# Kernel tuning notes

Hardware: AMD Instinct MI355X
Metric: run time of the kernel (lower is better)

Reference implementation:

```python
import jax, jax.numpy as jnp
import numpy as np

N_NONZERO = 32      # n_nonzero_coefs
TAU = 0.01
LAMBDA_INIT = -5.0  # reg_coeff = softplus(lambda)


def setup_inputs() -> dict:
    key = jax.random.key(0)
    k1, k2 = jax.random.split(key)
    X = jax.random.normal(k1, (64, 1024, 1024), dtype=jnp.float32)
    y = jax.random.normal(k2, (64, 1024, 1), dtype=jnp.float32)
    return {"X": X, "y": y}


def _omp_fit_forward(X, y):
    # Faithful translation of fit() (omp with hard straight-through top-1)
    # followed by forward() reconstruction D @ coef.
    reg = jax.nn.softplus(jnp.asarray(LAMBDA_INIT, jnp.float32)).astype(X.dtype)
    B, L, A = X.shape
    ones = jnp.ones((B, L, 1), X.dtype)
    Dfull = jnp.concatenate([X, ones], axis=-1)   # [B, L, A+1] (bias column)
    D = Dfull[0]                                   # shared dictionary [L, A+1]
    n_atoms = A + 1
    y2 = y[:, :, 0]                                # [B, L]
    y_det = jax.lax.stop_gradient(y2)
    residuals = y_det
    # Cache selected_D columns incrementally: each column j is dict @ ret_j,
    # identical math to the original's full recompute every iteration.
    selD = jnp.zeros((B, L, N_NONZERO), X.dtype)
    idx_all = []
    nzW = None
    for i in range(N_NONZERO):
        proj = residuals @ D                                      # [B, A+1]
        soft = jax.nn.softmax(jnp.abs(proj) / TAU, axis=-1)
        idx = jnp.argmax(jnp.abs(proj), axis=-1)                  # detached indices
        onehot = jax.nn.one_hot(jnp.argmax(soft, axis=-1), n_atoms, dtype=X.dtype)
        ret = onehot - jax.lax.stop_gradient(soft) + soft         # straight-through
        new_col = ret @ D.T                                       # [B, L]
        selD = selD.at[:, :, i].set(new_col)
        Di = selD[:, :, :i + 1]                                   # [B, L, i+1]
        DTy = jnp.einsum('blk,bl->bk', Di, y2)[..., None]         # [B, i+1, 1]
        DTD = jnp.einsum('blk,blj->bkj', Di, Di) + reg * jnp.eye(i + 1, dtype=X.dtype)
        nzW = jnp.linalg.solve(DTD, DTy)                          # [B, i+1, 1]
        residuals = y_det - jnp.einsum('blk,bk->bl', Di, nzW[..., 0])
        idx_all.append(idx)
    indices = jnp.stack(idx_all, axis=1)                          # [B, K] int
    W = jnp.zeros((B, n_atoms), X.dtype).at[jnp.arange(B)[:, None], indices].set(nzW[..., 0])
    # forward(): bmm(dict_with_bias, coef)
    recon = jnp.einsum('bla,ba->bl', Dfull, W)[..., None]         # [B, L, 1]
    return recon


def reference(X, y):
    return _omp_fit_forward(X, y)
```

## Files before the change

kernel.cpp:

```cpp
#include <hip/hip_runtime.h>
#include <math.h>

#define NATOMS   1025
#define GSTRIDE  1040
#define GELEMS   (1025*GSTRIDE)
#define NNZ      32
#define NBATCH   64
#define REGL     0.0067153485f

#define DPPF(x, ctrl) __int_as_float(__builtin_amdgcn_update_dpp(0, __float_as_int(x), (ctrl), 0xF, 0xF, false))

__device__ __forceinline__ float wave_max64(float x) {
    x = fmaxf(x, DPPF(x, 0x111));
    x = fmaxf(x, DPPF(x, 0x112));
    x = fmaxf(x, DPPF(x, 0x114));
    x = fmaxf(x, DPPF(x, 0x118));
    x = fmaxf(x, DPPF(x, 0x142));
    x = fmaxf(x, DPPF(x, 0x143));
    return __int_as_float(__builtin_amdgcn_readlane(__float_as_int(x), 63));
}
__device__ __forceinline__ float wave_sum64(float x) {
    x += DPPF(x, 0x111);
    x += DPPF(x, 0x112);
    x += DPPF(x, 0x114);
    x += DPPF(x, 0x118);
    x += DPPF(x, 0x142);
    x += DPPF(x, 0x143);
    return __int_as_float(__builtin_amdgcn_readlane(__float_as_int(x), 63));
}
__device__ __forceinline__ float readlane_f(float x, int l) {
    return __int_as_float(__builtin_amdgcn_readlane(__float_as_int(x), l));
}

__global__ __launch_bounds__(256)
void gramprojy_kernel(const float* __restrict__ X0, const float* __restrict__ y,
                      float* __restrict__ Gout, float* __restrict__ PY,
                      int kLen, int nsplit) {
    __shared__ float lds[8192];
    const int tid = threadIdx.x;

    if ((int)blockIdx.z < nsplit) {
        const int bx = blockIdx.x, by = blockIdx.y, bz = blockIdx.z;
        if (by < bx) return;
        float* As = lds;
        float* Bs = lds + 4096;
        const int a0 = bx * 128, b0 = by * 128;
        float* __restrict__ Gp = Gout + (size_t)bz * GELEMS;
        const int tx = tid & 15;
        const int ty = tid >> 4;
        const int lr = tid >> 5;
        const int lc = (tid & 31) * 4;
        const bool aIn = (a0 + 128) <= 1024;
        const bool bIn = (b0 + 128) <= 1024;

        float acc[8][8];
#pragma unroll
        for (int m = 0; m < 8; ++m)
#pragma unroll
            for (int n = 0; n < 8; ++n) acc[m][n] = 0.0f;

        const int kBase = bz * kLen;
        for (int kc = 0; kc < kLen; kc += 32) {
#pragma unroll
            for (int rr = 0; rr < 4; ++rr) {
                const int r = lr + rr * 8;
                const int l = kBase + kc + r;
                if (aIn) {
                    *(float4*)&As[r * 128 + lc] = *(const float4*)&X0[(size_t)l * 1024 + a0 + lc];
                } else {
#pragma unroll
                    for (int k = 0; k < 4; ++k) {
                        const int col = a0 + lc + k;
                        As[r * 128 + lc + k] = (col < 1024) ? X0[(size_t)l * 1024 + col]
                                                            : (col == 1024 ? 1.0f : 0.0f);
                    }
                }
                if (bIn) {
                    *(float4*)&Bs[r * 128 + lc] = *(const float4*)&X0[(size_t)l * 1024 + b0 + lc];
                } else {
#pragma unroll
                    for (int k = 0; k < 4; ++k) {
                        const int col = b0 + lc + k;
                        Bs[r * 128 + lc + k] = (col < 1024) ? X0[(size_t)l * 1024 + col]
                                                            : (col == 1024 ? 1.0f : 0.0f);
                    }
                }
            }
            __syncthreads();
#pragma unroll 8
            for (int l = 0; l < 32; ++l) {
                float4 a01 = *(const float4*)&As[l * 128 + ty * 8];
                float4 a23 = *(const float4*)&As[l * 128 + ty * 8 + 4];
                float4 bA  = *(const float4*)&Bs[l * 128 + tx * 4];
                float4 bB  = *(const float4*)&Bs[l * 128 + 64 + tx * 4];
                float am[8] = {a01.x, a01.y, a01.z, a01.w, a23.x, a23.y, a23.z, a23.w};
                float bn[8] = {bA.x, bA.y, bA.z, bA.w, bB.x, bB.y, bB.z, bB.w};
#pragma unroll
                for (int m = 0; m < 8; ++m)
#pragma unroll
                    for (int n = 0; n < 8; ++n)
                        acc[m][n] += am[m] * bn[n];
            }
            __syncthreads();
        }

#pragma unroll
        for (int m = 0; m < 8; ++m) {
            const int a = a0 + ty * 8 + m;
            if (a >= NATOMS) continue;
            const int bAc = b0 + tx * 4;
            const int bBc = b0 + 64 + tx * 4;
            if (bAc < GSTRIDE) {
                *(float4*)&Gp[(size_t)a * GSTRIDE + bAc] =
                    make_float4(acc[m][0], acc[m][1], acc[m][2], acc[m][3]);
            }
            if (bBc < GSTRIDE) {
                *(float4*)&Gp[(size_t)a * GSTRIDE + bBc] =
                    make_float4(acc[m][4], acc[m][5], acc[m][6], acc[m][7]);
            }
        }
        if (bx != by) {
#pragma unroll
            for (int n = 0; n < 8; ++n) {
                const int colg = b0 + ((n < 4) ? (tx * 4 + n) : (64 + tx * 4 + (n - 4)));
                if (colg >= NATOMS) continue;
                const int a = a0 + ty * 8;
                *(float4*)&Gp[(size_t)colg * GSTRIDE + a] =
                    make_float4(acc[0][n], acc[1][n], acc[2][n], acc[3][n]);
                *(float4*)&Gp[(size_t)colg * GSTRIDE + a + 4] =
                    make_float4(acc[4][n], acc[5][n], acc[6][n], acc[7][n]);
            }
        }
    } else {
        const int pw = blockIdx.y * 9 + blockIdx.x;
        if (pw >= 68) return;
        const int a0 = (pw % 17) * 64;
        const int b0 = (pw / 17) * 16;
        float* Ds = lds;
        float* Ys = lds + 2048;
        const int tx = tid & 15;
        const int ty = tid >> 4;
        const bool aIn = (a0 + 64) <= 1024;

        float acc[4] = {0.0f, 0.0f, 0.0f, 0.0f};

        for (int kc = 0; kc < 1024; kc += 32) {
            {
                const int r  = tid >> 4;
                const int c4 = (tid & 15) * 4;
#pragma unroll
                for (int rr = 0; rr < 2; ++rr) {
                    const int row = r + rr * 16;
                    const int l = kc + row;
                    if (aIn) {
                        *(float4*)&Ds[row * 64 + c4] = *(const float4*)&X0[(size_t)l * 1024 + a0 + c4];
                    } else {
#pragma unroll
                        for (int k = 0; k < 4; ++k) {
                            const int col = a0 + c4 + k;
                            Ds[row * 64 + c4 + k] = (col < 1024) ? X0[(size_t)l * 1024 + col]
                                                                 : (col == 1024 ? 1.0f : 0.0f);
                        }
                    }
                }
            }
            for (int e = tid; e < 512; e += 256) {
                const int l = e & 31, bb = e >> 5;
                Ys[l * 17 + bb] = y[(size_t)(b0 + bb) * 1024 + kc + l];
            }
            __syncthreads();
#pragma unroll 8
            for (int l = 0; l < 32; ++l) {
                const float yv = Ys[l * 17 + ty];
                float4 dv = *(const float4*)&Ds[l * 64 + tx * 4];
                acc[0] += yv * dv.x; acc[1] += yv * dv.y;
                acc[2] += yv * dv.z; acc[3] += yv * dv.w;
            }
            __syncthreads();
        }
        const int a = a0 + tx * 4;
        if (a < GSTRIDE) {
            *(float4*)&PY[(size_t)(b0 + ty) * GSTRIDE + a] =
                make_float4(acc[0], acc[1], acc[2], acc[3]);
        }
    }
}

template <int NS>
__global__ __launch_bounds__(512)
void omp_kernel(const float* __restrict__ Gp, const float* __restrict__ PY,
                int* __restrict__ idxOut, float* __restrict__ wOut) {
    __shared__ float pyLds[1040];
    __shared__ float diagLds[1040];
    __shared__ float bvec[32];
    __shared__ float row1024[NNZ];
    __shared__ float redV[2][8];
    __shared__ int   redI[2][8];

    const int b = blockIdx.x, tid = threadIdx.x;
    const int lane = tid & 63, wid = tid >> 6;

    float rr0[NNZ], rr1[NNZ];
    float ainv[32];
#pragma unroll
    for (int m = 0; m < 32; ++m) { ainv[m] = 0.f; rr0[m] = 0.f; rr1[m] = 0.f; }
    float wvr = 0.f, rhsr = 0.f;
    int   myIdx = 0;

    {
        const float* pyg = PY + (size_t)b * GSTRIDE;
        pyLds[tid] = pyg[tid];
        pyLds[tid + 512] = pyg[tid + 512];
        if (tid < 16) pyLds[1024 + tid] = pyg[1024 + tid];
        float d0 = 0.f, d1 = 0.f, d2 = 0.f;
#pragma unroll
        for (int z = 0; z < NS; ++z) {
            const float* gz = Gp + (size_t)z * GELEMS;
            d0 += gz[(size_t)tid * (GSTRIDE + 1)];
            d1 += gz[(size_t)(tid + 512) * (GSTRIDE + 1)];
            if (tid == 511) d2 += gz[(size_t)1024 * (GSTRIDE + 1)];
        }
        diagLds[tid] = d0;
        diagLds[tid + 512] = d1;
        if (tid == 511) diagLds[1024] = d2;
        if (tid < 32) { bvec[tid] = 0.f; row1024[tid] = 0.f; }
    }
    __syncthreads();

    float p0 = pyLds[tid], p1 = pyLds[tid + 512];
    float p2 = (tid == 511) ? pyLds[1024] : 0.f;

    {
        float best = fabsf(p0); int bidx = tid;
        { float v = fabsf(p1); if (v > best) { best = v; bidx = tid + 512; } }
        if (tid == 511) { float v = fabsf(p2); if (v > best) { best = v; bidx = 1024; } }
        const float wmax = wave_max64(best);
        const unsigned long long mask = __ballot(best == wmax);
        const int fl = __ffsll((unsigned long long)mask) - 1;
        const int widx = __builtin_amdgcn_readlane(bidx, fl);
        if (lane == 0) { redV[0][wid] = wmax; redI[0][wid] = widx; }
    }
    __syncthreads();

#define OMP_ITER(I)                                                            \
    {                                                                          \
        const int par = (I) & 1;                                               \
        float bv_ = redV[par][0]; int sel = redI[par][0];                      \
        _Pragma("unroll")                                                      \
        for (int q = 1; q < 8; ++q) {                                          \
            if (redV[par][q] > bv_ ||                                          \
                (redV[par][q] == bv_ && redI[par][q] < sel)) {                 \
                bv_ = redV[par][q]; sel = redI[par][q];                        \
            }                                                                  \
        }                                                                      \
        const float pysel = pyLds[sel];                                        \
        float rA0=0.f,rA1=0.f,rA2=0.f,rA3=0.f;                                 \
        float rB0=0.f,rB1=0.f,rB2=0.f,rB3=0.f,rC=0.f;                          \
        if ((I) < NNZ - 1) {                                                   \
            const size_t ro = (size_t)sel * GSTRIDE;                           \
            { const float* g = Gp + ro; rA0 = g[tid]; rB0 = g[tid + 512]; }    \
            if (NS > 1) { const float* g = Gp + ro + (size_t)1 * GELEMS;       \
                          rA1 = g[tid]; rB1 = g[tid + 512]; }                  \
            if (NS > 2) { const float* g = Gp + ro + (size_t)2 * GELEMS;       \
                          rA2 = g[tid]; rB2 = g[tid + 512]; }                  \
            if (NS > 3) { const float* g = Gp + ro + (size_t)3 * GELEMS;       \
                          rA3 = g[tid]; rB3 = g[tid + 512]; }                  \
            if (tid == 511) {                                                  \
                _Pragma("unroll")                                              \
                for (int z = 0; z < NS; ++z)                                   \
                    rC += Gp[(size_t)z * GELEMS + ro + 1024];                  \
            }                                                                  \
        }                                                                      \
        if (sel == 1024) {                                                     \
            if (tid < 32) bvec[tid] = row1024[tid];                            \
        } else if (tid == (sel & 511)) {                                       \
            if (sel >> 9) {                                                    \
                _Pragma("unroll")                                              \
                for (int m = 0; m < 32; ++m) bvec[m] = rr1[m];                 \
            } else {                                                           \
                _Pragma("unroll")                                              \
                for (int m = 0; m < 32; ++m) bvec[m] = rr0[m];                 \
            }                                                                  \
        }                                                                      \
        __syncthreads();                               \
        const float bvl = (lane < 32) ? bvec[lane] : 0.f;                      \
        float u0 = 0.f, u1 = 0.f;                                              \
        _Pragma("unroll")                                                      \
        for (int m = 0; m < 32; m += 2) {                                      \
            u0 = fmaf(ainv[m],     bvec[m],     u0);                           \
            u1 = fmaf(ainv[m + 1], bvec[m + 1], u1);                           \
        }                                                                      \
        const float uacc = u0 + u1;                                            \
        const float t = wave_sum64(bvl * uacc);                                \
        const float s = wave_sum64(rhsr * uacc);                               \
        const float dinv = 1.0f / (diagLds[sel] + REGL - t);                   \
        const float beta = dinv * (pysel - s);                                 \
        const float uvb = (lane == (I)) ? -1.0f : uacc;                        \
        _Pragma("unroll")                                                      \
        for (int m = 0; m < 32; ++m)                                           \
            ainv[m] = fmaf(uvb * dinv, readlane_f(uvb, m), ainv[m]);           \
        wvr  = (lane == (I)) ? beta  : fmaf(-uacc, beta, wvr);                 \
        rhsr = (lane == (I)) ? pysel : rhsr;                                   \
        if (tid == (I)) myIdx = sel;                                           \
        if ((I) < NNZ - 1) {                                                   \
            float z0 = 0.f, z1 = 0.f, z2 = 0.f;                                \
            _Pragma("unroll")                                                  \
            for (int j = 0; j < NNZ - 1; ++j) {                                \
                if (j < (I)) {                                                 \
                    const float uj = readlane_f(uvb, j);                       \
                    z0 = fmaf(uj, rr0[j], z0);                                 \
                    z1 = fmaf(uj, rr1[j], z1);                                 \
                    if (tid == 511) z2 = fmaf(uj, row1024[j], z2);             \
                }                                                              \
            }                                                                  \
            const float r0 = (rA0 + rA1) + (rA2 + rA3);                        \
            const float r1 = (rB0 + rB1) + (rB2 + rB3);                        \
            p0 = fmaf(beta, z0, p0); p0 = fmaf(-beta, r0, p0);                 \
            p1 = fmaf(beta, z1, p1); p1 = fmaf(-beta, r1, p1);                 \
            if (tid == 511) { p2 = fmaf(beta, z2, p2);                         \
                              p2 = fmaf(-beta, rC, p2); }                      \
            rr0[(I)] = r0; rr1[(I)] = r1;                                      \
            if (tid == 511) row1024[(I)] = rC;                                 \
            float best = fabsf(p0); int bidx = tid;                            \
            { float v = fabsf(p1); if (v > best) { best = v; bidx = tid + 512; } } \
            if (tid == 511) { float v = fabsf(p2);                             \
                              if (v > best) { best = v; bidx = 1024; } }       \
            const float wmax = wave_max64(best);                               \
            const unsigned long long mask = __ballot(best == wmax);            \
            const int fl = __ffsll((unsigned long long)mask) - 1;              \
            const int widx = __builtin_amdgcn_readlane(bidx, fl);              \
            if (lane == 0) { redV[par ^ 1][wid] = wmax;                        \
                             redI[par ^ 1][wid] = widx; }                      \
            __syncthreads();                    \
        }                                                                      \
    }

    OMP_ITER(0)  OMP_ITER(1)  OMP_ITER(2)  OMP_ITER(3)
    OMP_ITER(4)  OMP_ITER(5)  OMP_ITER(6)  OMP_ITER(7)
    OMP_ITER(8)  OMP_ITER(9)  OMP_ITER(10) OMP_ITER(11)
    OMP_ITER(12) OMP_ITER(13) OMP_ITER(14) OMP_ITER(15)
    OMP_ITER(16) OMP_ITER(17) OMP_ITER(18) OMP_ITER(19)
    OMP_ITER(20) OMP_ITER(21) OMP_ITER(22) OMP_ITER(23)
    OMP_ITER(24) OMP_ITER(25) OMP_ITER(26) OMP_ITER(27)
    OMP_ITER(28) OMP_ITER(29) OMP_ITER(30) OMP_ITER(31)
#undef OMP_ITER

    if (tid < NNZ) {
        idxOut[b * NNZ + tid] = myIdx;
        wOut[b * NNZ + tid] = wvr;
    }
}

__global__ __launch_bounds__(256)
void recon_kernel(const float* __restrict__ X, const int* __restrict__ idxIn,
                  const float* __restrict__ wIn, float* __restrict__ out) {
    __shared__ float Wd[1025];
    __shared__ float wval[NNZ];
    __shared__ int   widx[NNZ];
    __shared__ float biasS;
    const int b = blockIdx.x >> 2, chunk = blockIdx.x & 3;
    const int tid = threadIdx.x;
    for (int u = tid; u < 1025; u += 256) Wd[u] = 0.0f;
    __syncthreads();
    if (tid == 0) {
#pragma unroll
        for (int i = 0; i < NNZ; ++i) Wd[idxIn[b * NNZ + i]] = wIn[b * NNZ + i];
        float bias = 0.0f;
#pragma unroll
        for (int i = 0; i < NNZ; ++i) {
            const int gi = idxIn[b * NNZ + i];
            const float v = Wd[gi];
            Wd[gi] = 0.0f;
            const bool isOnes = (gi == 1024);
            if (isOnes) bias += v;
            widx[i] = isOnes ? 0 : gi;
            wval[i] = isOnes ? 0.0f : v;
        }
        biasS = bias;
    }
    __syncthreads();
    const int l = chunk * 256 + tid;
    const float* __restrict__ xr = X + (size_t)b * 1024 * 1024 + (size_t)l * 1024;
    float a0 = biasS, a1 = 0.f, a2 = 0.f, a3 = 0.f;
#pragma unroll
    for (int i = 0; i < NNZ; i += 4) {
        a0 = fmaf(xr[widx[i + 0]], wval[i + 0], a0);
        a1 = fmaf(xr[widx[i + 1]], wval[i + 1], a1);
        a2 = fmaf(xr[widx[i + 2]], wval[i + 2], a2);
        a3 = fmaf(xr[widx[i + 3]], wval[i + 3], a3);
    }
    out[(size_t)b * 1024 + l] = (a0 + a1) + (a2 + a3);
}

extern "C" void kernel_launch(void* const* d_in, const int* in_sizes, int n_in,
                              void* d_out, int out_size, void* d_ws, size_t ws_size,
                              hipStream_t stream) {
    const float* X = (const float*)d_in[0];
    const float* y = (const float*)d_in[1];
    float* out = (float*)d_out;
    float* ws = (float*)d_ws;

    const size_t fixed = (size_t)64 * GSTRIDE + NBATCH * NNZ * 2 + 64;
    const size_t need4 = ((size_t)GELEMS * 4 + fixed) * sizeof(float);
    const int nsplit = (ws_size >= need4) ? 4 : 1;
    const int kLen = 1024 / nsplit;

    float* Gp = ws;
    float* PY = ws + (size_t)GELEMS * nsplit;
    float* wOut = PY + (size_t)64 * GSTRIDE;
    int* idxOut = (int*)(wOut + NBATCH * NNZ);

    gramprojy_kernel<<<dim3(9, 9, nsplit + 1), 256, 0, stream>>>(X, y, Gp, PY, kLen, nsplit);
    if (nsplit == 4) omp_kernel<4><<<NBATCH, 512, 0, stream>>>(Gp, PY, idxOut, wOut);
    else             omp_kernel<1><<<NBATCH, 512, 0, stream>>>(Gp, PY, idxOut, wOut);
    recon_kernel<<<NBATCH * 4, 256, 0, stream>>>(X, idxOut, wOut, out);
}
```

Baseline: 179.8 us.

## Cache selected Gram columns in LDS, fuse argmax reduction, dense-read recon

The OMP kernel now keeps a transposed LDS table holding every atom's Gram-column history, so the selected column is read directly. This removes the per-iteration bvec broadcast and one __syncthreads. The wave argmax now carries value and index together through DPP steps instead of using a max, ballot and readlane sequence. The recon kernel no longer gathers 32 scattered entries per row; it reads full X rows with float4 coalesced loads and does a wave-sum dot against a dense weight vector. This moves 4x more bytes of X but with coalesced access, and the colT array takes about 135KB of LDS, which could limit occupancy.

```diff
diff --git a/kernel.cpp b/kernel.cpp
--- a/kernel.cpp
+++ b/kernel.cpp
@@ -4,21 +4,13 @@
 #define NATOMS   1025
 #define GSTRIDE  1040
 #define GELEMS   (1025*GSTRIDE)
+#define CSTRIDE  33
 #define NNZ      32
 #define NBATCH   64
 #define REGL     0.0067153485f
 
 #define DPPF(x, ctrl) __int_as_float(__builtin_amdgcn_update_dpp(0, __float_as_int(x), (ctrl), 0xF, 0xF, false))
 
-__device__ __forceinline__ float wave_max64(float x) {
-    x = fmaxf(x, DPPF(x, 0x111));
-    x = fmaxf(x, DPPF(x, 0x112));
-    x = fmaxf(x, DPPF(x, 0x114));
-    x = fmaxf(x, DPPF(x, 0x118));
-    x = fmaxf(x, DPPF(x, 0x142));
-    x = fmaxf(x, DPPF(x, 0x143));
-    return __int_as_float(__builtin_amdgcn_readlane(__float_as_int(x), 63));
-}
 __device__ __forceinline__ float wave_sum64(float x) {
     x += DPPF(x, 0x111);
     x += DPPF(x, 0x112);
@@ -190,10 +182,9 @@
 __global__ __launch_bounds__(512)
 void omp_kernel(const float* __restrict__ Gp, const float* __restrict__ PY,
                 int* __restrict__ idxOut, float* __restrict__ wOut) {
+    __shared__ float colT[NATOMS * CSTRIDE];
     __shared__ float pyLds[1040];
     __shared__ float diagLds[1040];
-    __shared__ float bvec[32];
-    __shared__ float row1024[NNZ];
     __shared__ float redV[2][8];
     __shared__ int   redI[2][8];
 
@@ -208,6 +199,7 @@
     int   myIdx = 0;
 
     {
+        for (int u = tid; u < NATOMS * CSTRIDE; u += 512) colT[u] = 0.f;
         const float* pyg = PY + (size_t)b * GSTRIDE;
         pyLds[tid] = pyg[tid];
         pyLds[tid + 512] = pyg[tid + 512];
@@ -223,22 +215,26 @@
         diagLds[tid] = d0;
         diagLds[tid + 512] = d1;
         if (tid == 511) diagLds[1024] = d2;
-        if (tid < 32) { bvec[tid] = 0.f; row1024[tid] = 0.f; }
     }
     __syncthreads();
 
     float p0 = pyLds[tid], p1 = pyLds[tid + 512];
     float p2 = (tid == 511) ? pyLds[1024] : 0.f;
 
+#define AM_STEP(ctrl) {                                                        \
+        float ov = DPPF(wv_, ctrl);                                            \
+        int   oi = __builtin_amdgcn_update_dpp(0, wi_, (ctrl), 0xF, 0xF, false);\
+        if (ov > wv_ || (ov == wv_ && oi < wi_)) { wv_ = ov; wi_ = oi; } }
     {
         float best = fabsf(p0); int bidx = tid;
         { float v = fabsf(p1); if (v > best) { best = v; bidx = tid + 512; } }
         if (tid == 511) { float v = fabsf(p2); if (v > best) { best = v; bidx = 1024; } }
-        const float wmax = wave_max64(best);
-        const unsigned long long mask = __ballot(best == wmax);
-        const int fl = __ffsll((unsigned long long)mask) - 1;
-        const int widx = __builtin_amdgcn_readlane(bidx, fl);
-        if (lane == 0) { redV[0][wid] = wmax; redI[0][wid] = widx; }
+        float wv_ = best; int wi_ = bidx;
+        AM_STEP(0x111) AM_STEP(0x112) AM_STEP(0x114) AM_STEP(0x118)
+        AM_STEP(0x142) AM_STEP(0x143)
+        wv_ = readlane_f(wv_, 63);
+        wi_ = __builtin_amdgcn_readlane(wi_, 63);
+        if (lane == 0) { redV[0][wid] = wv_; redI[0][wid] = wi_; }
     }
     __syncthreads();
 
@@ -271,24 +267,13 @@
                     rC += Gp[(size_t)z * GELEMS + ro + 1024];                  \
             }                                                                  \
         }                                                                      \
-        if (sel == 1024) {                                                     \
-            if (tid < 32) bvec[tid] = row1024[tid];                            \
-        } else if (tid == (sel & 511)) {                                       \
-            if (sel >> 9) {                                                    \
-                _Pragma("unroll")                                              \
-                for (int m = 0; m < 32; ++m) bvec[m] = rr1[m];                 \
-            } else {                                                           \
-                _Pragma("unroll")                                              \
-                for (int m = 0; m < 32; ++m) bvec[m] = rr0[m];                 \
-            }                                                                  \
-        }                                                                      \
-        __syncthreads();                               \
-        const float bvl = (lane < 32) ? bvec[lane] : 0.f;                      \
+        const float* csel = &colT[sel * CSTRIDE];                              \
+        const float bvl = (lane < 32) ? csel[lane] : 0.f;                      \
         float u0 = 0.f, u1 = 0.f;                                              \
         _Pragma("unroll")                                                      \
         for (int m = 0; m < 32; m += 2) {                                      \
-            u0 = fmaf(ainv[m],     bvec[m],     u0);                           \
-            u1 = fmaf(ainv[m + 1], bvec[m + 1], u1);                           \
+            u0 = fmaf(ainv[m],     csel[m],     u0);                           \
+            u1 = fmaf(ainv[m + 1], csel[m + 1], u1);                           \
         }                                                                      \
         const float uacc = u0 + u1;                                            \
         const float t = wave_sum64(bvl * uacc);                                \
@@ -310,7 +295,7 @@
                     const float uj = readlane_f(uvb, j);                       \
                     z0 = fmaf(uj, rr0[j], z0);                                 \
                     z1 = fmaf(uj, rr1[j], z1);                                 \
-                    if (tid == 511) z2 = fmaf(uj, row1024[j], z2);             \
+                    if (tid == 511) z2 = fmaf(uj, colT[1024 * CSTRIDE + j], z2); \
                 }                                                              \
             }                                                                  \
             const float r0 = (rA0 + rA1) + (rA2 + rA3);                        \
@@ -320,18 +305,21 @@
             if (tid == 511) { p2 = fmaf(beta, z2, p2);                         \
                               p2 = fmaf(-beta, rC, p2); }                      \
             rr0[(I)] = r0; rr1[(I)] = r1;                                      \
-            if (tid == 511) row1024[(I)] = rC;                                 \
+            colT[tid * CSTRIDE + (I)] = r0;                                    \
+            colT[(tid + 512) * CSTRIDE + (I)] = r1;                            \
+            if (tid == 511) colT[1024 * CSTRIDE + (I)] = rC;                   \
             float best = fabsf(p0); int bidx = tid;                            \
             { float v = fabsf(p1); if (v > best) { best = v; bidx = tid + 512; } } \
             if (tid == 511) { float v = fabsf(p2);                             \
                               if (v > best) { best = v; bidx = 1024; } }       \
-            const float wmax = wave_max64(best);                               \
-            const unsigned long long mask = __ballot(best == wmax);            \
-            const int fl = __ffsll((unsigned long long)mask) - 1;              \
-            const int widx = __builtin_amdgcn_readlane(bidx, fl);              \
-            if (lane == 0) { redV[par ^ 1][wid] = wmax;                        \
-                             redI[par ^ 1][wid] = widx; }                      \
-            __syncthreads();                    \
+            float wv_ = best; int wi_ = bidx;                                  \
+            AM_STEP(0x111) AM_STEP(0x112) AM_STEP(0x114) AM_STEP(0x118)       \
+            AM_STEP(0x142) AM_STEP(0x143)                                      \
+            wv_ = readlane_f(wv_, 63);                                         \
+            wi_ = __builtin_amdgcn_readlane(wi_, 63);                          \
+            if (lane == 0) { redV[par ^ 1][wid] = wv_;                         \
+                             redI[par ^ 1][wid] = wi_; }                       \
+            __syncthreads();                              \
         }                                                                      \
     }
 
@@ -344,6 +332,7 @@
     OMP_ITER(24) OMP_ITER(25) OMP_ITER(26) OMP_ITER(27)
     OMP_ITER(28) OMP_ITER(29) OMP_ITER(30) OMP_ITER(31)
 #undef OMP_ITER
+#undef AM_STEP
 
     if (tid < NNZ) {
         idxOut[b * NNZ + tid] = myIdx;
@@ -354,42 +343,33 @@
 __global__ __launch_bounds__(256)
 void recon_kernel(const float* __restrict__ X, const int* __restrict__ idxIn,
                   const float* __restrict__ wIn, float* __restrict__ out) {
-    __shared__ float Wd[1025];
-    __shared__ float wval[NNZ];
-    __shared__ int   widx[NNZ];
-    __shared__ float biasS;
-    const int b = blockIdx.x >> 2, chunk = blockIdx.x & 3;
-    const int tid = threadIdx.x;
-    for (int u = tid; u < 1025; u += 256) Wd[u] = 0.0f;
+    __shared__ float4 Wd4[260];
+    const int b = blockIdx.x >> 3, chunk = blockIdx.x & 7;
+    const int tid = threadIdx.x, lane = tid & 63, wid = tid >> 6;
+    float* Wd = (float*)Wd4;
+    for (int u = tid; u < 1040; u += 256) Wd[u] = 0.0f;
     __syncthreads();
     if (tid == 0) {
 #pragma unroll
         for (int i = 0; i < NNZ; ++i) Wd[idxIn[b * NNZ + i]] = wIn[b * NNZ + i];
-        float bias = 0.0f;
-#pragma unroll
-        for (int i = 0; i < NNZ; ++i) {
-            const int gi = idxIn[b * NNZ + i];
-            const float v = Wd[gi];
-            Wd[gi] = 0.0f;
-            const bool isOnes = (gi == 1024);
-            if (isOnes) bias += v;
-            widx[i] = isOnes ? 0 : gi;
-            wval[i] = isOnes ? 0.0f : v;
-        }
-        biasS = bias;
     }
     __syncthreads();
-    const int l = chunk * 256 + tid;
-    const float* __restrict__ xr = X + (size_t)b * 1024 * 1024 + (size_t)l * 1024;
-    float a0 = biasS, a1 = 0.f, a2 = 0.f, a3 = 0.f;
-#pragma unroll
-    for (int i = 0; i < NNZ; i += 4) {
-        a0 = fmaf(xr[widx[i + 0]], wval[i + 0], a0);
-        a1 = fmaf(xr[widx[i + 1]], wval[i + 1], a1);
-        a2 = fmaf(xr[widx[i + 2]], wval[i + 2], a2);
-        a3 = fmaf(xr[widx[i + 3]], wval[i + 3], a3);
-    }
-    out[(size_t)b * 1024 + l] = (a0 + a1) + (a2 + a3);
+    const float wOne = Wd[1024];
+    const float* Xb = X + (size_t)b * 1024 * 1024;
+
+    for (int rr = wid; rr < 128; rr += 4) {
+        const int r = chunk * 128 + rr;
+        const float4* xr = (const float4*)(Xb + (size_t)r * 1024);
+        float acc = 0.0f;
+#pragma unroll
+        for (int q = 0; q < 4; ++q) {
+            float4 x = xr[q * 64 + lane];
+            float4 w = Wd4[q * 64 + lane];
+            acc += x.x * w.x + x.y * w.y + x.z * w.z + x.w * w.w;
+        }
+        acc = wave_sum64(acc);
+        if (lane == 0) out[(size_t)b * 1024 + r] = acc + wOne;
+    }
 }
 
 extern "C" void kernel_launch(void* const* d_in, const int* in_sizes, int n_in,
@@ -413,5 +393,5 @@
     gramprojy_kernel<<<dim3(9, 9, nsplit + 1), 256, 0, stream>>>(X, y, Gp, PY, kLen, nsplit);
     if (nsplit == 4) omp_kernel<4><<<NBATCH, 512, 0, stream>>>(Gp, PY, idxOut, wOut);
     else             omp_kernel<1><<<NBATCH, 512, 0, stream>>>(Gp, PY, idxOut, wOut);
-    recon_kernel<<<NBATCH * 4, 256, 0, stream>>>(X, idxOut, wOut, out);
-}
+    recon_kernel<<<NBATCH * 8, 256, 0, stream>>>(X, idxOut, wOut, out);
+}
```

Result: slower. 187.2 us (+4.1%).
